# Performance work log

Hardware: AMD Instinct MI355X
Metric: run time of the kernel (lower is better)

Reference implementation:

```python
import jax, jax.numpy as jnp
import numpy as np

D, B, E, O = 8, 16, 2048, 2048  # delays, batch, pre, post


def setup_inputs() -> dict:
    key = jax.random.key(0)
    k_w, k_mask, k_xd, k_dm, k_ws, k_sp = jax.random.split(key, 6)
    # W = connectivity mask * magnitudes (sparse non-negative weights, buffer wmax folded in)
    conn = jax.random.bernoulli(k_mask, 0.1, (E, O)).astype(jnp.float32)
    W = jax.random.uniform(k_w, (E, O), dtype=jnp.float32) * 0.02 * conn
    # Delayed presynaptic spikes: sparse binary
    Xd = jax.random.bernoulli(k_xd, 0.02, (D, B, E)).astype(jnp.float32)
    # delaymap: binary (delay, pre, post) routing map, typically ~1 active delay per synapse
    delaymap = jax.random.bernoulli(k_dm, 0.125, (D, E, O)).astype(jnp.float32)
    # STP modulation (output of shortterm module, before the +1 offset)
    Wshort = (jax.random.uniform(k_ws, (D, B, E), dtype=jnp.float32) - 0.5) * 0.4
    # Per-presynaptic-neuron signs in {-1,+1}, stored as int
    signs_pre = jax.random.randint(k_sp, (E,), 0, 2, dtype=jnp.int32)
    return {"W": W, "Xd": Xd, "delaymap": delaymap, "Wshort": Wshort,
            "signs_pre": signs_pre}


def reference(W, Xd, delaymap, Wshort, signs_pre):
    # align_signs(): signs = signs_pre broadcast over post, zeroed where W <= 0
    s = (2 * signs_pre - 1).astype(W.dtype)  # map {0,1} -> {-1,+1}
    signs = jnp.where(W > 0, s[:, None], jnp.zeros((), W.dtype))  # (E, O)
    Ws = signs * W  # signed weights 'eo'
    # has_STP path: I = einsum('eo,dbe,deo,dbe->bo', W, Xd, delaymap, Wshort+1)
    I = jnp.einsum('eo,dbe,deo,dbe->bo', Ws, Xd, delaymap, Wshort + 1.0)
    return I
```

## Files before the change

### kernel.cpp

```cpp
#include <hip/hip_runtime.h>


constexpr int D = 8, B = 16, E = 2048, O = 2048;
constexpr int DB = D * B;
constexpr int OTILE = 512;
constexpr int THREADS2 = OTILE / 4;
constexpr int ESPLIT = 4;
constexpr int ECHUNK = E / ESPLIT;
constexpr int NSLICE = D * ESPLIT;

struct Entry { int e; float c; };

__global__ __launch_bounds__(128) void build_lists(
    const float* __restrict__ Xd, const float* __restrict__ Wshort,
    const int* __restrict__ signs, int* __restrict__ counts,
    Entry* __restrict__ entries)
{
    const int db   = blockIdx.x;
    const int part = blockIdx.y;
    const int e0   = part * ECHUNK;
    __shared__ int cnt;
    if (threadIdx.x == 0) cnt = 0;
    __syncthreads();
    const float4* __restrict__ xrow = (const float4*)(Xd + (size_t)db * E + e0);
    const float4* __restrict__ wsr  = (const float4*)(Wshort + (size_t)db * E + e0);
    Entry* __restrict__ out = entries + (size_t)db * E + e0;
    const int q = threadIdx.x;
    float4 x = xrow[q];
    if (x.x != 0.f || x.y != 0.f || x.z != 0.f || x.w != 0.f) {
        float4 ws = wsr[q];
        const float xa[4] = {x.x, x.y, x.z, x.w};
        const float wa[4] = {ws.x, ws.y, ws.z, ws.w};
        #pragma unroll
        for (int k = 0; k < 4; ++k) {
            if (xa[k] != 0.f) {
                int e = e0 + q * 4 + k;
                float s = (float)(2 * signs[e] - 1);
                float c = xa[k] * s * (1.0f + wa[k]);
                int slot = atomicAdd(&cnt, 1);
                out[slot].e = e;
                out[slot].c = c;
            }
        }
    }
    __syncthreads();
    if (threadIdx.x == 0) counts[db * ESPLIT + part] = cnt;
}

__global__ __launch_bounds__(THREADS2) void accum(
    const float* __restrict__ W, const float* __restrict__ dm,
    const int* __restrict__ counts, const Entry* __restrict__ entries,
    float* __restrict__ partial)
{
    const int tile = blockIdx.x;
    const int part = blockIdx.y;
    const int db   = blockIdx.z;
    const int d = db >> 4;
    const int b = db & 15;
    const int o0 = tile * OTILE + (int)threadIdx.x * 4;

    const int m = counts[db * ESPLIT + part];
    const Entry* __restrict__ lst = entries + (size_t)db * E + part * ECHUNK;

    const float* __restrict__ Wt  = W  + o0;
    const float* __restrict__ dmd = dm + (size_t)d * E * O + o0;
    float4 acc = make_float4(0.f, 0.f, 0.f, 0.f);
    #pragma unroll 4
    for (int j = 0; j < m; ++j) {
        Entry en = lst[j];
        const float4 w  = *(const float4*)(Wt  + (size_t)en.e * O);
        const float4 mm = *(const float4*)(dmd + (size_t)en.e * O);
        acc.x += en.c * w.x * mm.x;
        acc.y += en.c * w.y * mm.y;
        acc.z += en.c * w.z * mm.z;
        acc.w += en.c * w.w * mm.w;
    }

    float* p = partial + ((size_t)(d * ESPLIT + part) * B + b) * O + o0;
    *(float4*)p = acc;
}

__global__ __launch_bounds__(128) void reduce_slices(
    const float* __restrict__ partial, float* __restrict__ Iout)
{
    const int q = blockIdx.x * 128 + threadIdx.x;
    const float2* __restrict__ p = (const float2*)partial;
    float2 s = make_float2(0.f, 0.f);
    #pragma unroll
    for (int k = 0; k < NSLICE; ++k) {
        float2 v = p[(size_t)k * (B * O / 2) + q];
        s.x += v.x; s.y += v.y;
    }
    ((float2*)Iout)[q] = s;
}

extern "C" void kernel_launch(void* const* d_in, const int* in_sizes, int n_in,
                              void* d_out, int out_size, void* d_ws, size_t ws_size,
                              hipStream_t stream) {
    const float* W     = (const float*)d_in[0];
    const float* Xd    = (const float*)d_in[1];
    const float* dm    = (const float*)d_in[2];
    const float* Wsh   = (const float*)d_in[3];
    const int*   signs = (const int*)d_in[4];
    float* Iout = (float*)d_out;

    int*   counts  = (int*)d_ws;
    Entry* entries = (Entry*)((char*)d_ws + 4096);
    float* partial = (float*)((char*)d_ws + (4u << 20));

    build_lists<<<dim3(DB, ESPLIT), dim3(128), 0, stream>>>(Xd, Wsh, signs, counts, entries);
    dim3 grid(O / OTILE, ESPLIT, DB);
    accum<<<grid, dim3(THREADS2), 0, stream>>>(W, dm, counts, entries, partial);
    reduce_slices<<<dim3(B * O / (128 * 2)), dim3(128), 0, stream>>>(partial, Iout);
}
```

Baseline: 193.7 us.

## Fuse spike-list building into accumulation kernel using shared-memory lists

Merges the list-building kernel into the accumulation kernel. Each block now compacts its own nonzero presynaptic entries into shared memory, so the entry list no longer round-trips through global memory and one kernel launch disappears. The block shape also changes: each block is now 512 threads covering the full output width, instead of 128-thread blocks over 512-column tiles. This cuts the grid fourfold and gives each block more columns per gathered W/delaymap row, at the cost of fewer blocks to spread across the CUs.

Result: no change. 191.1 us (-1.3%).

```diff
diff --git a/kernel.cpp b/kernel.cpp
--- a/kernel.cpp
+++ b/kernel.cpp
@@ -3,71 +3,60 @@
 
 constexpr int D = 8, B = 16, E = 2048, O = 2048;
 constexpr int DB = D * B;
-constexpr int OTILE = 512;
-constexpr int THREADS2 = OTILE / 4;
 constexpr int ESPLIT = 4;
 constexpr int ECHUNK = E / ESPLIT;
 constexpr int NSLICE = D * ESPLIT;
+constexpr int THREADS2 = 512;
 
 struct Entry { int e; float c; };
 
-__global__ __launch_bounds__(128) void build_lists(
+__global__ __launch_bounds__(THREADS2) void accum_fused(
+    const float* __restrict__ W, const float* __restrict__ dm,
     const float* __restrict__ Xd, const float* __restrict__ Wshort,
-    const int* __restrict__ signs, int* __restrict__ counts,
-    Entry* __restrict__ entries)
+    const int* __restrict__ signs, float* __restrict__ partial)
 {
-    const int db   = blockIdx.x;
-    const int part = blockIdx.y;
-    const int e0   = part * ECHUNK;
+    const int part = blockIdx.x;
+    const int db   = blockIdx.y;
+    const int d = db >> 4;
+    const int b = db & 15;
+    const int e0 = part * ECHUNK;
+
     __shared__ int cnt;
+    __shared__ Entry sh[ECHUNK];
     if (threadIdx.x == 0) cnt = 0;
     __syncthreads();
-    const float4* __restrict__ xrow = (const float4*)(Xd + (size_t)db * E + e0);
-    const float4* __restrict__ wsr  = (const float4*)(Wshort + (size_t)db * E + e0);
-    Entry* __restrict__ out = entries + (size_t)db * E + e0;
-    const int q = threadIdx.x;
-    float4 x = xrow[q];
-    if (x.x != 0.f || x.y != 0.f || x.z != 0.f || x.w != 0.f) {
-        float4 ws = wsr[q];
-        const float xa[4] = {x.x, x.y, x.z, x.w};
-        const float wa[4] = {ws.x, ws.y, ws.z, ws.w};
-        #pragma unroll
-        for (int k = 0; k < 4; ++k) {
-            if (xa[k] != 0.f) {
-                int e = e0 + q * 4 + k;
-                float s = (float)(2 * signs[e] - 1);
-                float c = xa[k] * s * (1.0f + wa[k]);
-                int slot = atomicAdd(&cnt, 1);
-                out[slot].e = e;
-                out[slot].c = c;
+
+    if (threadIdx.x < ECHUNK / 4) {
+        const int q = threadIdx.x;
+        float4 x = ((const float4*)(Xd + (size_t)db * E + e0))[q];
+        if (x.x != 0.f || x.y != 0.f || x.z != 0.f || x.w != 0.f) {
+            float4 ws = ((const float4*)(Wshort + (size_t)db * E + e0))[q];
+            int4   sg = ((const int4*)(signs + e0))[q];
+            const float xa[4] = {x.x, x.y, x.z, x.w};
+            const float wa[4] = {ws.x, ws.y, ws.z, ws.w};
+            const int   sa[4] = {sg.x, sg.y, sg.z, sg.w};
+            #pragma unroll
+            for (int k = 0; k < 4; ++k) {
+                if (xa[k] != 0.f) {
+                    float s = (float)(2 * sa[k] - 1);
+                    float c = xa[k] * s * (1.0f + wa[k]);
+                    int slot = atomicAdd(&cnt, 1);
+                    sh[slot].e = e0 + q * 4 + k;
+                    sh[slot].c = c;
+                }
             }
         }
     }
     __syncthreads();
-    if (threadIdx.x == 0) counts[db * ESPLIT + part] = cnt;
-}
+    const int m = cnt;
 
-__global__ __launch_bounds__(THREADS2) void accum(
-    const float* __restrict__ W, const float* __restrict__ dm,
-    const int* __restrict__ counts, const Entry* __restrict__ entries,
-    float* __restrict__ partial)
-{
-    const int tile = blockIdx.x;
-    const int part = blockIdx.y;
-    const int db   = blockIdx.z;
-    const int d = db >> 4;
-    const int b = db & 15;
-    const int o0 = tile * OTILE + (int)threadIdx.x * 4;
-
-    const int m = counts[db * ESPLIT + part];
-    const Entry* __restrict__ lst = entries + (size_t)db * E + part * ECHUNK;
-
+    const int o0 = (int)threadIdx.x * 4;
     const float* __restrict__ Wt  = W  + o0;
     const float* __restrict__ dmd = dm + (size_t)d * E * O + o0;
     float4 acc = make_float4(0.f, 0.f, 0.f, 0.f);
     #pragma unroll 4
     for (int j = 0; j < m; ++j) {
-        Entry en = lst[j];
+        Entry en = sh[j];
         const float4 w  = *(const float4*)(Wt  + (size_t)en.e * O);
         const float4 mm = *(const float4*)(dmd + (size_t)en.e * O);
         acc.x += en.c * w.x * mm.x;
@@ -104,12 +93,9 @@
     const int*   signs = (const int*)d_in[4];
     float* Iout = (float*)d_out;
 
-    int*   counts  = (int*)d_ws;
-    Entry* entries = (Entry*)((char*)d_ws + 4096);
-    float* partial = (float*)((char*)d_ws + (4u << 20));
+    float* partial = (float*)d_ws;
 
-    build_lists<<<dim3(DB, ESPLIT), dim3(128), 0, stream>>>(Xd, Wsh, signs, counts, entries);
-    dim3 grid(O / OTILE, ESPLIT, DB);
-    accum<<<grid, dim3(THREADS2), 0, stream>>>(W, dm, counts, entries, partial);
+    accum_fused<<<dim3(ESPLIT, DB), dim3(THREADS2), 0, stream>>>(
+        W, dm, Xd, Wsh, signs, partial);
     reduce_slices<<<dim3(B * O / (128 * 2)), dim3(128), 0, stream>>>(partial, Iout);
 }
```
